# Kernel tuning notes

Hardware: AMD Instinct MI355X
Metric: run time of the kernel (lower is better)

The kernel has to match this reference:

```python
import jax, jax.numpy as jnp
import numpy as np

D_IN = 4096
NUM_LATENTS = 65536
GROUP_DIM = 64
GROUP_MUL = 4
IN_GROUPS = D_IN // GROUP_DIM      # 64
OUT_GROUPS = NUM_LATENTS // GROUP_DIM  # 1024
TOKENS = 2048


def setup_inputs() -> dict:
    key = jax.random.key(0)
    k1, k2, k3, k4, k5 = jax.random.split(key, 5)
    x = jax.random.normal(k1, (TOKENS, D_IN), dtype=jnp.float32)
    # nn.Linear default init ~ U(-1/sqrt(d), 1/sqrt(d)); scale randn similarly for stability
    s = 1.0 / np.sqrt(D_IN)
    pre_w = jax.random.normal(k2, (D_IN, D_IN), dtype=jnp.float32) * s
    pre_b = jax.random.normal(k3, (D_IN,), dtype=jnp.float32) * s
    inner = jax.random.normal(k4, (GROUP_MUL, IN_GROUPS, GROUP_DIM, GROUP_DIM), dtype=jnp.float32)
    outer = jax.random.normal(k5, (OUT_GROUPS, GROUP_MUL, IN_GROUPS), dtype=jnp.float32)
    return {"x": x, "pre_w": pre_w, "pre_b": pre_b, "inner": inner, "outer": outer}


def reference(x, pre_w, pre_b, inner, outer):
    # pre: dense linear, x @ W^T + b  -> (tokens, d_in)
    h = x @ pre_w.T + pre_b
    # unflatten last dim into (in_groups, group_dim)
    h = h.reshape(h.shape[0], IN_GROUPS, GROUP_DIM)  # (b, i, x)
    # block-diagonal mix: (b,i,x) x (m,i,x,y) -> (b,m,i,y)
    t = jnp.einsum('bix,mixy->bmiy', h, inner)
    # low-rank outer combine: (b,m,i,y) x (o,m,i) -> (b,o,y)
    out = jnp.einsum('bmiy,omi->boy', t, outer)
    # flatten (o, y) -> num_latents; note: module's _bias is unused in forward
    return out.reshape(out.shape[0], NUM_LATENTS)
```

## Files before the change

### kernel.cpp

```cpp
#include <hip/hip_runtime.h>
#include <hip/hip_bf16.h>
#include <stdint.h>

#define D_IN 4096
#define TOKENS 2048
#define NUM_LATENTS 65536
#define GROUP_MUL 4
#define IN_GROUPS 64
#define KMID 256

typedef __attribute__((ext_vector_type(8))) short short8;
typedef __attribute__((ext_vector_type(4))) float f32x4;

struct alignas(8)  US4 { unsigned short v[4]; };

#define FLAT_BLOCKS 24832

__device__ inline unsigned short f2bf(float f) {
    union { float f; unsigned u; } w{f};
    unsigned r = w.u + 0x7fffu + ((w.u >> 16) & 1u);
    return (unsigned short)(r >> 16);
}

__device__ inline void gload_lds16(const void* g, void* l) {
    __builtin_amdgcn_global_load_lds(
        (const __attribute__((address_space(1))) void*)g,
        (__attribute__((address_space(3))) void*)l, 16, 0, 0);
}

__device__ inline int SWZ(int y, int k) {
    return ((y << 9) + (k << 1)) ^ ((((y & 7) ^ ((y >> 3) & 7)) << 4));
}

__global__ __launch_bounds__(256) void cvt_all(
    const float* __restrict__ w, const float* __restrict__ x,
    const float* __restrict__ outer, const float* __restrict__ inner,
    unsigned short* __restrict__ w_bf, unsigned short* __restrict__ x_bf,
    unsigned short* __restrict__ o_bf, unsigned short* __restrict__ it_bf) {
    __shared__ float tl[64][65];
    int blk = blockIdx.x;
    const int tid = threadIdx.x;
    if (blk >= FLAT_BLOCKS) {
        blk -= FLAT_BLOCKS;
        const float* src = inner + (size_t)blk * 4096;
        #pragma unroll
        for (int p = 0; p < 4; ++p) {
            int idx = p * 1024 + tid * 4;
            int xx = idx >> 6, y = idx & 63;
            f32x4 v = *(const f32x4*)(src + idx);
            #pragma unroll
            for (int j = 0; j < 4; ++j) tl[xx][y + j] = v[j];
        }
        __syncthreads();
        unsigned short* dst = it_bf + (size_t)blk * 4096;
        #pragma unroll
        for (int p = 0; p < 4; ++p) {
            int idx = p * 1024 + tid * 4;
            int y = idx >> 6, x0 = idx & 63;
            US4 o;
            #pragma unroll
            for (int j = 0; j < 4; ++j) o.v[j] = f2bf(tl[x0 + j][y]);
            *(US4*)(dst + y * 64 + (x0 ^ ((y & 7) << 3))) = o;
        }
        return;
    }
    int s = blk * 256 + tid;
    if (s < 4194304) {
        f32x4 v = *(const f32x4*)(w + (size_t)s * 4);
        US4 o;
        #pragma unroll
        for (int j = 0; j < 4; ++j) o.v[j] = f2bf(v[j]);
        *(US4*)(w_bf + (size_t)s * 4) = o;
    } else if (s < 6291456) {
        int t = s - 4194304;
        f32x4 v = *(const f32x4*)(x + (size_t)t * 4);
        US4 o;
        #pragma unroll
        for (int j = 0; j < 4; ++j) o.v[j] = f2bf(v[j]);
        *(US4*)(x_bf + (size_t)t * 4) = o;
    } else {
        int t0 = (s - 6291456) * 4;
        int o = t0 >> 8, r = t0 & 255, m = r >> 6, i = r & 63;
        f32x4 v = *(const f32x4*)(outer + t0);
        #pragma unroll
        for (int j = 0; j < 4; ++j)
            o_bf[(o << 8) + (i + j) * 4 + m] = f2bf(v[j]);
    }
}

__global__ __launch_bounds__(512, 2) void gemm_fused(
    const unsigned short* __restrict__ A,
    const unsigned short* __restrict__ B,
    const float* __restrict__ bias,
    const unsigned short* __restrict__ IT,
    unsigned short* __restrict__ T)
{
    __shared__ unsigned short smem[49152];

    const int tid = threadIdx.x;
    const int lane = tid & 63;
    const int w = tid >> 6;
    const int wm = w >> 2;
    const int wn = w & 3;
    int bx = blockIdx.x;
    const int logical = (bx & 7) * 32 + (bx >> 3);
    const int m0 = (logical & 15) * 128;
    const int n0 = (logical >> 4) * 256;
    const int i0 = n0 >> 6;

    const int lr = lane & 15;
    const int hi = lane >> 4;
    const int lk = hi * 8;

    f32x4 acc[4][4] = {};

    auto STAGE_A = [&](unsigned short* As, int k0) {
        #pragma unroll
        for (int c = 0; c < 2; ++c) {
            int f = c * 4096 + tid * 8;
            int r = f >> 6;
            int colsw = ((((f >> 3) & 7) ^ (r & 7)) << 3);
            gload_lds16(A + (size_t)(m0 + r) * D_IN + k0 + colsw, As + f);
        }
    };
    auto STAGE_B = [&](unsigned short* Bs, int k0, int c0) {
        #pragma unroll
        for (int c = 0; c < 2; ++c) {
            int f = (c0 + c) * 4096 + tid * 8;
            int r = f >> 6;
            int colsw = ((((f >> 3) & 7) ^ (r & 7)) << 3);
            gload_lds16(B + (size_t)(n0 + r) * D_IN + k0 + colsw, Bs + f);
        }
    };

    STAGE_A(smem, 0);
    STAGE_B(smem + 8192, 0, 0);
    STAGE_B(smem + 8192, 0, 2);

    short8 a0, a1, a2, a3, b0, b1, b2, b3;
    #define RD_A(dst, mi, kk, as) { int row = wm * 64 + (mi) * 16 + lr; \
        dst = *(const short8*)((as) + (row << 6) + ((((kk << 2) + hi) ^ (lr & 7)) << 3)); }
    #define RD_B(dst, ni, kk, bs) { int row = wn * 64 + (ni) * 16 + lr; \
        dst = *(const short8*)((bs) + (row << 6) + ((((kk << 2) + hi) ^ (lr & 7)) << 3)); }
    #define MF(mi, ni, bb, aa) acc[mi][ni] = __builtin_amdgcn_mfma_f32_16x16x32_bf16(bb, aa, acc[mi][ni], 0, 0, 0);
    #define PHASE_TAIL \
        __builtin_amdgcn_s_barrier(); \
        asm volatile("s_waitcnt lgkmcnt(0)" ::: "memory"); \
        __builtin_amdgcn_sched_barrier(0);
    #define PHASE_END \
        __builtin_amdgcn_s_setprio(0); \
        __builtin_amdgcn_s_barrier(); \
        __builtin_amdgcn_sched_barrier(0);

    #pragma unroll 1
    for (int t = 0; t < 64; ++t) {
        unsigned short* As = smem + (t & 1) * 24576;
        unsigned short* Bs = As + 8192;
        unsigned short* Asn = smem + ((t & 1) ^ 1) * 24576;
        unsigned short* Bsn = Asn + 8192;
        const int kn = (t + 1) * 64;

        asm volatile("s_waitcnt vmcnt(0)" ::: "memory");
        __builtin_amdgcn_s_barrier();
        __builtin_amdgcn_sched_barrier(0);

        if (t < 63) STAGE_A(Asn, kn);
        RD_A(a0, 0, 0, As) RD_A(a1, 1, 0, As) RD_A(a2, 2, 0, As) RD_A(a3, 3, 0, As)
        RD_B(b0, 0, 0, Bs) RD_B(b1, 1, 0, Bs)
        PHASE_TAIL
        __builtin_amdgcn_s_setprio(1);
        MF(0,0,b0,a0) MF(1,0,b0,a1) MF(2,0,b0,a2) MF(3,0,b0,a3)
        MF(0,1,b1,a0) MF(1,1,b1,a1) MF(2,1,b1,a2) MF(3,1,b1,a3)
        PHASE_END

        if (t < 63) STAGE_B(Bsn, kn, 0);
        RD_B(b2, 2, 0, Bs) RD_B(b3, 3, 0, Bs)
        PHASE_TAIL
        __builtin_amdgcn_s_setprio(1);
        MF(0,2,b2,a0) MF(1,2,b2,a1) MF(2,2,b2,a2) MF(3,2,b2,a3)
        MF(0,3,b3,a0) MF(1,3,b3,a1) MF(2,3,b3,a2) MF(3,3,b3,a3)
        PHASE_END

        if (t < 63) STAGE_B(Bsn, kn, 2);
        RD_A(a0, 0, 1, As) RD_A(a1, 1, 1, As) RD_A(a2, 2, 1, As) RD_A(a3, 3, 1, As)
        RD_B(b0, 0, 1, Bs) RD_B(b1, 1, 1, Bs)
        PHASE_TAIL
        __builtin_amdgcn_s_setprio(1);
        MF(0,0,b0,a0) MF(1,0,b0,a1) MF(2,0,b0,a2) MF(3,0,b0,a3)
        MF(0,1,b1,a0) MF(1,1,b1,a1) MF(2,1,b1,a2) MF(3,1,b1,a3)
        PHASE_END

        RD_B(b2, 2, 1, Bs) RD_B(b3, 3, 1, Bs)
        PHASE_TAIL
        __builtin_amdgcn_s_setprio(1);
        MF(0,2,b2,a0) MF(1,2,b2,a1) MF(2,2,b2,a2) MF(3,2,b2,a3)
        MF(0,3,b3,a0) MF(1,3,b3,a1) MF(2,3,b3,a2) MF(3,3,b3,a3)
        PHASE_END
    }

    #pragma unroll
    for (int ni = 0; ni < 4; ++ni) {
        int col0 = wn * 64 + ni * 16 + hi * 4;
        f32x4 bv = *(const f32x4*)(bias + n0 + col0);
        #pragma unroll
        for (int mi = 0; mi < 4; ++mi) {
            int tok = wm * 64 + mi * 16 + lr;
            US4 o;
            #pragma unroll
            for (int j = 0; j < 4; ++j) o.v[j] = f2bf(acc[mi][ni][j] + bv[j]);
            *(US4*)(smem + tok * 256 + (col0 ^ ((tok & 7) << 3))) = o;
        }
    }

    unsigned short* inn = smem + 32768;
    for (int m = 0; m < 4; ++m) {
        #pragma unroll
        for (int c = 0; c < 4; ++c) {
            int e = c * 4096 + tid * 8;
            int i_l = e >> 12, rem = e & 4095;
            gload_lds16(IT + ((size_t)(m * 64 + i0 + i_l) << 12) + rem, inn + e);
        }
        asm volatile("s_waitcnt vmcnt(0)" ::: "memory");
        __syncthreads();

        f32x4 acc2[4][4] = {};
        #pragma unroll
        for (int kk = 0; kk < 2; ++kk) {
            short8 a[4], b2v[4];
            #pragma unroll
            for (int mi = 0; mi < 4; ++mi) {
                int tok = wm * 64 + mi * 16 + lr;
                a[mi] = *(const short8*)(smem + tok * 256 + ((wn * 64 + kk * 32 + lk) ^ ((tok & 7) << 3)));
            }
            #pragma unroll
            for (int ni = 0; ni < 4; ++ni) {
                int y = ni * 16 + lr;
                b2v[ni] = *(const short8*)(inn + wn * 4096 + y * 64 + ((kk * 32 + lk) ^ ((y & 7) << 3)));
            }
            #pragma unroll
            for (int mi = 0; mi < 4; ++mi)
                #pragma unroll
                for (int ni = 0; ni < 4; ++ni)
                    acc2[mi][ni] = __builtin_amdgcn_mfma_f32_16x16x32_bf16(b2v[ni], a[mi], acc2[mi][ni], 0, 0, 0);
        }

        const int kp = (i0 + wn) * 4 + m;
        #pragma unroll
        for (int mi = 0; mi < 4; ++mi) {
            int tok = m0 + wm * 64 + mi * 16 + lr;
            unsigned short* trow = T + ((size_t)tok * KMID + kp) * 64;
            #pragma unroll
            for (int ni = 0; ni < 4; ++ni) {
                int y0 = ni * 16 + hi * 4;
                US4 o;
                #pragma unroll
                for (int j = 0; j < 4; ++j) o.v[j] = f2bf(acc2[mi][ni][j]);
                *(US4*)(trow + y0) = o;
            }
        }
        __syncthreads();
    }
    #undef RD_A
    #undef RD_B
    #undef MF
    #undef PHASE_TAIL
    #undef PHASE_END
}

__global__ __launch_bounds__(512) void stage3(
    const unsigned short* __restrict__ T,
    const unsigned short* __restrict__ Ob,
    float* __restrict__ out)
{
    __shared__ char ts[32768];
    const int tid = threadIdx.x;
    const int lane = tid & 63;
    const int w = tid >> 6;
    int bx = blockIdx.x;
    const int b = (bx & 7) * 256 + (bx >> 3);
    const int lr = lane & 15;
    const int hi = lane >> 4;

    {
        const unsigned short* src = T + (size_t)b * (KMID * 64);
        #pragma unroll
        for (int c = 0; c < 4; ++c) {
            int e = c * 4096 + tid * 8;
            int k = e >> 6, y = e & 63;
            short8 v = __builtin_nontemporal_load((const short8*)(src + e));
            #pragma unroll
            for (int j = 0; j < 8; ++j)
                *(unsigned short*)(ts + SWZ(y + j, k)) = (unsigned short)v[j];
        }
    }
    __syncthreads();

    const int o_base = w * 128;
    f32x4 acc[4][8] = {};
    for (int kt = 0; kt < 8; ++kt) {
        short8 tf[4], of[8];
        #pragma unroll
        for (int ni = 0; ni < 4; ++ni)
            tf[ni] = *(const short8*)(ts + SWZ(ni * 16 + lr, kt * 32 + hi * 8));
        #pragma unroll
        for (int mi = 0; mi < 8; ++mi)
            of[mi] = *(const short8*)(Ob + ((size_t)(o_base + mi * 16 + lr) << 8) + kt * 32 + hi * 8);
        #pragma unroll
        for (int ni = 0; ni < 4; ++ni)
            #pragma unroll
            for (int mi = 0; mi < 8; ++mi)
                acc[ni][mi] = __builtin_amdgcn_mfma_f32_16x16x32_bf16(tf[ni], of[mi], acc[ni][mi], 0, 0, 0);
    }

    float* ob = out + (size_t)b * NUM_LATENTS;
    #pragma unroll
    for (int ni = 0; ni < 4; ++ni) {
        #pragma unroll
        for (int mi = 0; mi < 8; ++mi) {
            int o = o_base + mi * 16 + lr;
            int y = ni * 16 + hi * 4;
            __builtin_nontemporal_store(acc[ni][mi], (f32x4*)(ob + (o << 6) + y));
        }
    }
}

extern "C" void kernel_launch(void* const* d_in, const int* in_sizes, int n_in,
                              void* d_out, int out_size, void* d_ws, size_t ws_size,
                              hipStream_t stream) {
    const float* x     = (const float*)d_in[0];
    const float* pre_w = (const float*)d_in[1];
    const float* pre_b = (const float*)d_in[2];
    const float* inner = (const float*)d_in[3];
    const float* outer = (const float*)d_in[4];
    float* out = (float*)d_out;

    char* ws = (char*)d_ws;
    unsigned short* x_bf = (unsigned short*)ws;  ws += (size_t)TOKENS * D_IN * 2;
    unsigned short* w_bf = (unsigned short*)ws;  ws += (size_t)D_IN * D_IN * 2;
    unsigned short* o_bf = (unsigned short*)ws;  ws += (size_t)1024 * KMID * 2;
    unsigned short* t_bf = (unsigned short*)ws;  ws += (size_t)TOKENS * KMID * 64 * 2;
    unsigned short* it_bf = (unsigned short*)ws; ws += (size_t)GROUP_MUL * IN_GROUPS * 64 * 64 * 2;

    cvt_all<<<FLAT_BLOCKS + GROUP_MUL * IN_GROUPS, 256, 0, stream>>>(
        pre_w, x, outer, inner, w_bf, x_bf, o_bf, it_bf);

    gemm_fused<<<256, 512, 0, stream>>>(x_bf, w_bf, pre_b, it_bf, t_bf);
    stage3<<<2048, 512, 0, stream>>>(t_bf, o_bf, out);
}
```

Before: 315.4 us.

## Make stage3 persistent over eight tokens with double-buffered LDS prefetch

Stage3 now launches 256 blocks, and each block handles eight tokens in sequence instead of one token per block. The next token's T tile is loaded into registers while the current one computes, then written into a second LDS buffer, so the global load overlaps with MFMA work and stores. The aim is to hide load latency and cut block launch overhead. In exchange, occupancy drops to one 512-thread block per CU with 64KB of LDS, only 256 blocks are in flight, and the kt loop is no longer unrolled, which may reduce parallelism for this store-bound kernel.

```diff
diff --git a/kernel.cpp b/kernel.cpp
--- a/kernel.cpp
+++ b/kernel.cpp
@@ -267,59 +267,91 @@
     #undef PHASE_END
 }
 
-__global__ __launch_bounds__(512) void stage3(
+__global__ __launch_bounds__(512, 1) void stage3(
     const unsigned short* __restrict__ T,
     const unsigned short* __restrict__ Ob,
     float* __restrict__ out)
 {
-    __shared__ char ts[32768];
+    __shared__ char ts[65536];
     const int tid = threadIdx.x;
     const int lane = tid & 63;
     const int w = tid >> 6;
-    int bx = blockIdx.x;
-    const int b = (bx & 7) * 256 + (bx >> 3);
+    const int bx = blockIdx.x;
+    const int b0 = ((bx & 7) * 32 + (bx >> 3)) * 8;
     const int lr = lane & 15;
     const int hi = lane >> 4;
-
+    const int o_base = w * 128;
+
+    short8 pre[4];
     {
-        const unsigned short* src = T + (size_t)b * (KMID * 64);
+        const unsigned short* src = T + (size_t)b0 * (KMID * 64);
+        #pragma unroll
+        for (int c = 0; c < 4; ++c)
+            pre[c] = __builtin_nontemporal_load((const short8*)(src + c * 4096 + tid * 8));
         #pragma unroll
         for (int c = 0; c < 4; ++c) {
             int e = c * 4096 + tid * 8;
             int k = e >> 6, y = e & 63;
-            short8 v = __builtin_nontemporal_load((const short8*)(src + e));
             #pragma unroll
             for (int j = 0; j < 8; ++j)
-                *(unsigned short*)(ts + SWZ(y + j, k)) = (unsigned short)v[j];
+                *(unsigned short*)(ts + SWZ(y + j, k)) = (unsigned short)pre[c][j];
         }
     }
     __syncthreads();
 
-    const int o_base = w * 128;
-    f32x4 acc[4][8] = {};
-    for (int kt = 0; kt < 8; ++kt) {
-        short8 tf[4], of[8];
-        #pragma unroll
-        for (int ni = 0; ni < 4; ++ni)
-            tf[ni] = *(const short8*)(ts + SWZ(ni * 16 + lr, kt * 32 + hi * 8));
-        #pragma unroll
-        for (int mi = 0; mi < 8; ++mi)
-            of[mi] = *(const short8*)(Ob + ((size_t)(o_base + mi * 16 + lr) << 8) + kt * 32 + hi * 8);
-        #pragma unroll
-        for (int ni = 0; ni < 4; ++ni)
+    int cur = 0;
+    #pragma unroll 1
+    for (int it = 0; it < 8; ++it) {
+        const int b = b0 + it;
+
+        if (it < 7) {
+            const unsigned short* src = T + (size_t)(b + 1) * (KMID * 64);
+            #pragma unroll
+            for (int c = 0; c < 4; ++c)
+                pre[c] = __builtin_nontemporal_load((const short8*)(src + c * 4096 + tid * 8));
+        }
+
+        const char* tsc = ts + cur * 32768;
+        f32x4 acc[4][8] = {};
+        #pragma unroll 1
+        for (int kt = 0; kt < 8; ++kt) {
+            short8 tf[4], of[8];
+            #pragma unroll
+            for (int ni = 0; ni < 4; ++ni)
+                tf[ni] = *(const short8*)(tsc + SWZ(ni * 16 + lr, kt * 32 + hi * 8));
             #pragma unroll
             for (int mi = 0; mi < 8; ++mi)
-                acc[ni][mi] = __builtin_amdgcn_mfma_f32_16x16x32_bf16(tf[ni], of[mi], acc[ni][mi], 0, 0, 0);
-    }
-
-    float* ob = out + (size_t)b * NUM_LATENTS;
-    #pragma unroll
-    for (int ni = 0; ni < 4; ++ni) {
-        #pragma unroll
-        for (int mi = 0; mi < 8; ++mi) {
-            int o = o_base + mi * 16 + lr;
-            int y = ni * 16 + hi * 4;
-            __builtin_nontemporal_store(acc[ni][mi], (f32x4*)(ob + (o << 6) + y));
+                of[mi] = *(const short8*)(Ob + ((size_t)(o_base + mi * 16 + lr) << 8) + kt * 32 + hi * 8);
+            #pragma unroll
+            for (int ni = 0; ni < 4; ++ni)
+                #pragma unroll
+                for (int mi = 0; mi < 8; ++mi)
+                    acc[ni][mi] = __builtin_amdgcn_mfma_f32_16x16x32_bf16(tf[ni], of[mi], acc[ni][mi], 0, 0, 0);
+        }
+
+        float* ob = out + (size_t)b * NUM_LATENTS;
+        #pragma unroll
+        for (int ni = 0; ni < 4; ++ni) {
+            #pragma unroll
+            for (int mi = 0; mi < 8; ++mi) {
+                int o = o_base + mi * 16 + lr;
+                int y = ni * 16 + hi * 4;
+                __builtin_nontemporal_store(acc[ni][mi], (f32x4*)(ob + (o << 6) + y));
+            }
+        }
+
+        if (it < 7) {
+            char* tsn = ts + (cur ^ 1) * 32768;
+            #pragma unroll
+            for (int c = 0; c < 4; ++c) {
+                int e = c * 4096 + tid * 8;
+                int k = e >> 6, y = e & 63;
+                #pragma unroll
+                for (int j = 0; j < 8; ++j)
+                    *(unsigned short*)(tsn + SWZ(y + j, k)) = (unsigned short)pre[c][j];
+            }
+            __syncthreads();
+            cur ^= 1;
         }
     }
 }
@@ -345,5 +377,5 @@
         pre_w, x, outer, inner, w_bf, x_bf, o_bf, it_bf);
 
     gemm_fused<<<256, 512, 0, stream>>>(x_bf, w_bf, pre_b, it_bf, t_bf);
-    stage3<<<2048, 512, 0, stream>>>(t_bf, o_bf, out);
-}
+    stage3<<<256, 512, 0, stream>>>(t_bf, o_bf, out);
+}
```

Result: no change. 313.8 us (-0.5%).
